# Kernel tuning notes

Hardware: AMD Instinct MI355X
Metric: run time of the kernel (lower is better)

The kernel has to match this reference:

```python
import jax, jax.numpy as jnp
import numpy as np
from jax import lax

MEL = 80
HID = 512
NCLS = 64
B = 16
T = 1000


def setup_inputs() -> dict:
    key = jax.random.key(0)
    ks = jax.random.split(key, 16)
    s_in = 1.0 / np.sqrt(MEL)
    s_h = 1.0 / np.sqrt(HID)
    return {
        'feats': jax.random.normal(ks[0], (B, T, MEL), jnp.float32),
        'C0': jax.random.normal(ks[1], (MEL, HID), jnp.float32) * s_h,
        'B0': jax.random.normal(ks[2], (HID, MEL), jnp.float32) * s_in,
        'W0': jax.random.normal(ks[3], (HID, MEL), jnp.float32) * s_in,
        'a0': jax.random.normal(ks[4], (HID,), jnp.float32) * 0.1,
        'tau00': jnp.array([0.5], jnp.float32),
        'gamma0': jnp.array([0.25], jnp.float32),
        'C1': jax.random.normal(ks[5], (HID, HID), jnp.float32) * s_h,
        'B1': jax.random.normal(ks[6], (HID, HID), jnp.float32) * s_h,
        'W1': jax.random.normal(ks[7], (HID, HID), jnp.float32) * s_h,
        'a1': jax.random.normal(ks[8], (HID,), jnp.float32) * 0.1,
        'tau01': jnp.array([0.5], jnp.float32),
        'gamma1': jnp.array([0.25], jnp.float32),
        'head_w': jax.random.normal(ks[9], (NCLS, 2 * HID), jnp.float32) * (1.0 / np.sqrt(2 * HID)),
        'head_b': jnp.zeros((NCLS,), jnp.float32),
    }


def _cell_step(h, x_t, C, Bm, Wm, a, tau0, gamma):
    # x_t: (B, in_dim), h: (B, HID)
    x_scale = jnp.maximum(jnp.linalg.norm(x_t, axis=-1, keepdims=True), 1e-6)  # (B,1)
    x_norm = jnp.clip(x_t / x_scale, -1.0, 1.0)
    hd = lax.stop_gradient(h)
    error = x_t - jnp.tanh(hd @ C.T) * x_scale                                 # (B, in_dim)
    rel_err = jnp.minimum(jnp.linalg.norm(error, axis=-1) / lax.stop_gradient(x_scale[:, 0]), 4.0)
    surprise = jax.nn.sigmoid((rel_err - tau0[0]) / gamma[0])                   # (B,)
    base_eff = x_norm @ Bm.T                                                    # (B, HID)
    err_eff = error @ Wm.T                                                      # (B, HID)
    input_h = hd * 0.2 + base_eff * 0.6 + err_eff * surprise[:, None] * 0.2
    # liquid-time-constant update: surprise-gated leaky integration toward tanh(input_h)
    g = surprise[:, None] * jax.nn.sigmoid(a)[None, :]                          # (B, HID) in (0,1)
    h_new = h * (1.0 - g) + jnp.tanh(input_h) * g
    return h_new, base_eff


def reference(feats, C0, B0, W0, a0, tau00, gamma0, C1, B1, W1, a1, tau01, gamma1, head_w, head_b):
    Bsz = feats.shape[0]
    feats_t = jnp.swapaxes(feats, 0, 1)  # (T, B, MEL)
    h0_init = jnp.zeros((Bsz, HID), feats.dtype)
    h1_init = jnp.zeros((Bsz, HID), feats.dtype)

    def scan_fn(carry, x_t):
        h0, h1 = carry
        h0n, be0 = _cell_step(h0, x_t, C0, B0, W0, a0, tau00, gamma0)
        h1n, be1 = _cell_step(h1, be0, C1, B1, W1, a1, tau01, gamma1)
        return (h0n, h1n), jnp.concatenate([h1n, be1], axis=-1)

    _, ys = lax.scan(scan_fn, (h0_init, h1_init), feats_t)  # (T, B, 2*HID)
    stacked = jnp.swapaxes(ys, 0, 1)                        # (B, T, 2*HID)
    return stacked @ head_w.T + head_b                      # (B, T, NCLS)
```

## Files before the change

### kernel.cpp

```cpp
#include <hip/hip_runtime.h>
#include <math.h>

#define T_LEN 1000
#define BATCH 16
#define MEL   80
#define HID   512
#define NCLS  64
#define SL    8

__device__ __forceinline__ float fast_tanh(float x) {
    float e = __expf(2.0f * x);
    return 1.0f - 2.0f / (e + 1.0f);
}
__device__ __forceinline__ float fast_sigmoid(float x) {
    return 1.0f / (1.0f + __expf(-x));
}

__device__ __forceinline__ unsigned long long pack_pair(float v, unsigned e) {
    return ((unsigned long long)e << 32) | (unsigned long long)__float_as_uint(v);
}
__device__ __forceinline__ float pair_val(unsigned long long p) {
    return __uint_as_float((unsigned)(p & 0xffffffffull));
}
__device__ __forceinline__ unsigned pair_epoch(unsigned long long p) {
    return (unsigned)(p >> 32);
}

__device__ __forceinline__ void llc_load16c(const float* base, float4 (&r)[16]) {
    asm volatile(
        "global_load_dwordx4 %0, %16, off sc0 sc1\n\t"
        "global_load_dwordx4 %1, %16, off offset:16 sc0 sc1\n\t"
        "global_load_dwordx4 %2, %16, off offset:32 sc0 sc1\n\t"
        "global_load_dwordx4 %3, %16, off offset:48 sc0 sc1\n\t"
        "global_load_dwordx4 %4, %16, off offset:64 sc0 sc1\n\t"
        "global_load_dwordx4 %5, %16, off offset:80 sc0 sc1\n\t"
        "global_load_dwordx4 %6, %16, off offset:96 sc0 sc1\n\t"
        "global_load_dwordx4 %7, %16, off offset:112 sc0 sc1\n\t"
        "global_load_dwordx4 %8, %16, off offset:128 sc0 sc1\n\t"
        "global_load_dwordx4 %9, %16, off offset:144 sc0 sc1\n\t"
        "global_load_dwordx4 %10, %16, off offset:160 sc0 sc1\n\t"
        "global_load_dwordx4 %11, %16, off offset:176 sc0 sc1\n\t"
        "global_load_dwordx4 %12, %16, off offset:192 sc0 sc1\n\t"
        "global_load_dwordx4 %13, %16, off offset:208 sc0 sc1\n\t"
        "global_load_dwordx4 %14, %16, off offset:224 sc0 sc1\n\t"
        "global_load_dwordx4 %15, %16, off offset:240 sc0 sc1\n\t"
        "s_waitcnt vmcnt(0)"
        : "=&v"(r[0]), "=&v"(r[1]), "=&v"(r[2]), "=&v"(r[3]),
          "=&v"(r[4]), "=&v"(r[5]), "=&v"(r[6]), "=&v"(r[7]),
          "=&v"(r[8]), "=&v"(r[9]), "=&v"(r[10]), "=&v"(r[11]),
          "=&v"(r[12]), "=&v"(r[13]), "=&v"(r[14]), "=&v"(r[15])
        : "v"(base)
        : "memory");
}

#define PART_WORDS (BATCH * 2 * SL * HID)
__global__ void k0_init(unsigned long long* part) {
    int i = blockIdx.x * 256 + threadIdx.x;
    if (i < PART_WORDS) part[i] = 0ull;
}

__global__ __launch_bounds__(256) void k1_be0(const float* __restrict__ feats,
                                              const float* __restrict__ B0,
                                              float* __restrict__ be0) {
    const int t = blockIdx.x;
    const int tid = threadIdx.x;
    __shared__ float xf[BATCH][MEL];
    __shared__ float sc[BATCH];
    for (int idx = tid; idx < BATCH * MEL; idx += 256) {
        int b = idx / MEL, m = idx % MEL;
        xf[b][m] = feats[b * (T_LEN * MEL) + t * MEL + m];
    }
    __syncthreads();
    if (tid < BATCH) {
        float ss = 0.f;
        for (int m = 0; m < MEL; ++m) { float v = xf[tid][m]; ss += v * v; }
        sc[tid] = fmaxf(sqrtf(ss), 1e-6f);
    }
    __syncthreads();
    for (int idx = tid; idx < BATCH * MEL; idx += 256) {
        int b = idx / MEL, m = idx % MEL;
        float v = xf[b][m] / sc[b];
        xf[b][m] = fminf(fmaxf(v, -1.f), 1.f);
    }
    __syncthreads();
    for (int j = tid; j < HID; j += 256) {
        float acc[BATCH];
        #pragma unroll
        for (int b = 0; b < BATCH; ++b) acc[b] = 0.f;
        const float* brow = B0 + j * MEL;
        for (int k = 0; k < MEL; k += 4) {
            float4 w = *(const float4*)(brow + k);
            #pragma unroll
            for (int b = 0; b < BATCH; ++b) {
                float4 xv = *(const float4*)(&xf[b][k]);
                acc[b] += w.x * xv.x + w.y * xv.y + w.z * xv.z + w.w * xv.w;
            }
        }
        #pragma unroll
        for (int b = 0; b < BATCH; ++b)
            be0[(t * BATCH + b) * HID + j] = acc[b];
    }
}

__global__ __launch_bounds__(512, 1) void k3_fused(
    const float* __restrict__ be0g,
    const float* __restrict__ C1, const float* __restrict__ W1,
    const float* __restrict__ B1,
    const float* __restrict__ a1, const float* __restrict__ tau,
    const float* __restrict__ gam,
    float* __restrict__ be1g, float* __restrict__ h1s,
    unsigned long long* part)
{
    const int chain = blockIdx.x & 15;
    const int slice = blockIdx.x >> 4;
    const int tid = threadIdx.x;
    const int w = tid >> 6;
    const int lane = tid & 63;
    const int jq = tid >> 3;
    const int kc = tid & 7;
    const int j2 = slice * 64 + jq;
    const bool lead = (kc == 0);

    float4 wC[16], wW[16], wB[16];
    llc_load16c(C1 + (size_t)tid * HID + slice * 64, wC);
    llc_load16c(W1 + (size_t)j2 * HID + kc * 64, wW);
    llc_load16c(B1 + (size_t)j2 * HID + kc * 64, wB);

    const float tauv = tau[0], gamv = gam[0];
    const float siga = fast_sigmoid(a1[j2]);

    unsigned long long* pc = part + (size_t)chain * (2 * SL * HID);

    __shared__ float h_s[64];
    __shared__ __align__(16) float e_s[HID + 32];
    __shared__ __align__(16) float x_s[HID + 32];
    __shared__ float sq_s[8];
    __shared__ float xsq_s[8];

    float hj = 0.f;
    if (tid < 64) h_s[tid] = 0.f;

    float cur_be0 = be0g[(size_t)chain * HID + tid];
    float cur_xs, cur_be1 = 0.f;
    {
        float sq = cur_be0 * cur_be0;
        #pragma unroll
        for (int off = 32; off > 0; off >>= 1) sq += __shfl_down(sq, off, 64);
        if (lane == 0) xsq_s[w] = sq;
        __syncthreads();
        float ssX = ((xsq_s[0] + xsq_s[1]) + (xsq_s[2] + xsq_s[3]))
                  + ((xsq_s[4] + xsq_s[5]) + (xsq_s[6] + xsq_s[7]));
        cur_xs = fmaxf(sqrtf(ssX), 1e-6f);
        float xn = cur_be0 / cur_xs;
        x_s[tid + (tid >> 6) * 4] = fminf(fmaxf(xn, -1.f), 1.f);
        __syncthreads();
        const float* xb = x_s + kc * 68;
        float q0 = 0.f, q1 = 0.f, q2 = 0.f, q3 = 0.f;
        #pragma unroll
        for (int i = 0; i < 16; ++i) {
            float4 v4 = *(const float4*)(xb + 4 * i);
            q0 += wB[i].x * v4.x; q1 += wB[i].y * v4.y;
            q2 += wB[i].z * v4.z; q3 += wB[i].w * v4.w;
        }
        float bq = (q0 + q1) + (q2 + q3);
        bq += __shfl_down(bq, 4, 8);
        bq += __shfl_down(bq, 2, 8);
        bq += __shfl_down(bq, 1, 8);
        if (lead) {
            cur_be1 = bq;
            __builtin_nontemporal_store(bq, &be1g[(size_t)chain * HID + j2]);
        }
        __syncthreads();
    }

    for (int t = 0; t < T_LEN; ++t) {
        float nxt_be0 = 0.f;
        if (t + 1 < T_LEN)
            nxt_be0 = be0g[(size_t)((t + 1) * BATCH + chain) * HID + tid];
        const unsigned tag = (unsigned)(t + 1);
        unsigned long long* ps = pc + (size_t)(t & 1) * (SL * HID);

        {
            float p0 = 0.f, p1 = 0.f, p2 = 0.f, p3 = 0.f;
            #pragma unroll
            for (int i = 0; i < 16; ++i) {
                float4 hv = *(const float4*)(h_s + 4 * i);
                p0 += wC[i].x * hv.x; p1 += wC[i].y * hv.y;
                p2 += wC[i].z * hv.z; p3 += wC[i].w * hv.w;
            }
            float pp = (p0 + p1) + (p2 + p3);
            __hip_atomic_store(&ps[slice * HID + tid], pack_pair(pp, tag),
                               __ATOMIC_RELAXED, __HIP_MEMORY_SCOPE_AGENT);
        }

        float nxt_xs = 0.f, nxt_be1 = 0.f;
        if (t + 1 < T_LEN) {
            float sq = nxt_be0 * nxt_be0;
            #pragma unroll
            for (int off = 32; off > 0; off >>= 1) sq += __shfl_down(sq, off, 64);
            if (lane == 0) xsq_s[w] = sq;
            __syncthreads();
            float ssX = ((xsq_s[0] + xsq_s[1]) + (xsq_s[2] + xsq_s[3]))
                      + ((xsq_s[4] + xsq_s[5]) + (xsq_s[6] + xsq_s[7]));
            nxt_xs = fmaxf(sqrtf(ssX), 1e-6f);
            float xn = nxt_be0 / nxt_xs;
            x_s[tid + (tid >> 6) * 4] = fminf(fmaxf(xn, -1.f), 1.f);
            __syncthreads();
            const float* xb = x_s + kc * 68;
            float q0 = 0.f, q1 = 0.f, q2 = 0.f, q3 = 0.f;
            #pragma unroll
            for (int i = 0; i < 16; ++i) {
                float4 v4 = *(const float4*)(xb + 4 * i);
                q0 += wB[i].x * v4.x; q1 += wB[i].y * v4.y;
                q2 += wB[i].z * v4.z; q3 += wB[i].w * v4.w;
            }
            float bq = (q0 + q1) + (q2 + q3);
            bq += __shfl_down(bq, 4, 8);
            bq += __shfl_down(bq, 2, 8);
            bq += __shfl_down(bq, 1, 8);
            if (lead) {
                nxt_be1 = bq;
                __builtin_nontemporal_store(bq,
                    &be1g[(size_t)((t + 1) * BATCH + chain) * HID + j2]);
            }
        }

        float dp;
        {
            const unsigned long long* a0 = ps + 0 * HID + tid;
            const unsigned long long* a1p = ps + 1 * HID + tid;
            const unsigned long long* a2 = ps + 2 * HID + tid;
            const unsigned long long* a3 = ps + 3 * HID + tid;
            const unsigned long long* a4 = ps + 4 * HID + tid;
            const unsigned long long* a5 = ps + 5 * HID + tid;
            const unsigned long long* a6 = ps + 6 * HID + tid;
            const unsigned long long* a7 = ps + 7 * HID + tid;
            unsigned long long q0, q1, q2, q3, q4, q5, q6, q7;
            int rounds = 0;
            for (;;) {
                asm volatile(
                    "global_load_dwordx2 %0, %8, off sc0 sc1\n\t"
                    "global_load_dwordx2 %1, %9, off sc0 sc1\n\t"
                    "global_load_dwordx2 %2, %10, off sc0 sc1\n\t"
                    "global_load_dwordx2 %3, %11, off sc0 sc1\n\t"
                    "global_load_dwordx2 %4, %12, off sc0 sc1\n\t"
                    "global_load_dwordx2 %5, %13, off sc0 sc1\n\t"
                    "global_load_dwordx2 %6, %14, off sc0 sc1\n\t"
                    "global_load_dwordx2 %7, %15, off sc0 sc1\n\t"
                    "s_waitcnt vmcnt(0)"
                    : "=&v"(q0), "=&v"(q1), "=&v"(q2), "=&v"(q3),
                      "=&v"(q4), "=&v"(q5), "=&v"(q6), "=&v"(q7)
                    : "v"(a0), "v"(a1p), "v"(a2), "v"(a3),
                      "v"(a4), "v"(a5), "v"(a6), "v"(a7)
                    : "memory");
                bool ok = (pair_epoch(q0) == tag) & (pair_epoch(q1) == tag)
                        & (pair_epoch(q2) == tag) & (pair_epoch(q3) == tag)
                        & (pair_epoch(q4) == tag) & (pair_epoch(q5) == tag)
                        & (pair_epoch(q6) == tag) & (pair_epoch(q7) == tag);
                if (__all(ok)) break;
                if (++rounds > 200000) {
                    q0 = __hip_atomic_load(a0, __ATOMIC_RELAXED, __HIP_MEMORY_SCOPE_AGENT);
                    q1 = __hip_atomic_load(a1p, __ATOMIC_RELAXED, __HIP_MEMORY_SCOPE_AGENT);
                    q2 = __hip_atomic_load(a2, __ATOMIC_RELAXED, __HIP_MEMORY_SCOPE_AGENT);
                    q3 = __hip_atomic_load(a3, __ATOMIC_RELAXED, __HIP_MEMORY_SCOPE_AGENT);
                    q4 = __hip_atomic_load(a4, __ATOMIC_RELAXED, __HIP_MEMORY_SCOPE_AGENT);
                    q5 = __hip_atomic_load(a5, __ATOMIC_RELAXED, __HIP_MEMORY_SCOPE_AGENT);
                    q6 = __hip_atomic_load(a6, __ATOMIC_RELAXED, __HIP_MEMORY_SCOPE_AGENT);
                    q7 = __hip_atomic_load(a7, __ATOMIC_RELAXED, __HIP_MEMORY_SCOPE_AGENT);
                    bool ok2 = (pair_epoch(q0) == tag) & (pair_epoch(q1) == tag)
                             & (pair_epoch(q2) == tag) & (pair_epoch(q3) == tag)
                             & (pair_epoch(q4) == tag) & (pair_epoch(q5) == tag)
                             & (pair_epoch(q6) == tag) & (pair_epoch(q7) == tag);
                    if (__all(ok2)) break;
                    rounds = 0;
                }
                __builtin_amdgcn_s_sleep(1);
            }
            dp = ((pair_val(q0) + pair_val(q1)) + (pair_val(q2) + pair_val(q3)))
               + ((pair_val(q4) + pair_val(q5)) + (pair_val(q6) + pair_val(q7)));
        }

        {
            float err = cur_be0 - fast_tanh(dp) * cur_xs;
            e_s[tid + (tid >> 6) * 4] = err;
            float sq = err * err;
            #pragma unroll
            for (int off = 32; off > 0; off >>= 1) sq += __shfl_down(sq, off, 64);
            if (lane == 0) sq_s[w] = sq;
        }
        __syncthreads();

        {
            float ssT = ((sq_s[0] + sq_s[1]) + (sq_s[2] + sq_s[3]))
                      + ((sq_s[4] + sq_s[5]) + (sq_s[6] + sq_s[7]));
            const float* esb = e_s + kc * 68;
            float q0 = 0.f, q1 = 0.f, q2 = 0.f, q3 = 0.f;
            #pragma unroll
            for (int i = 0; i < 16; ++i) {
                float4 ev = *(const float4*)(esb + 4 * i);
                q0 += wW[i].x * ev.x; q1 += wW[i].y * ev.y;
                q2 += wW[i].z * ev.z; q3 += wW[i].w * ev.w;
            }
            float ee = (q0 + q1) + (q2 + q3);
            ee += __shfl_down(ee, 4, 8);
            ee += __shfl_down(ee, 2, 8);
            ee += __shfl_down(ee, 1, 8);
            if (lead) {
                float rel = fminf(sqrtf(ssT) / cur_xs, 4.0f);
                float s = fast_sigmoid((rel - tauv) / gamv);
                float input_h = hj * 0.2f + cur_be1 * 0.6f + ee * s * 0.2f;
                float g = s * siga;
                hj = hj * (1.f - g) + fast_tanh(input_h) * g;
                h_s[jq] = hj;
                __builtin_nontemporal_store(hj,
                    &h1s[(size_t)(t * BATCH + chain) * HID + j2]);
            }
        }
        __syncthreads();

        cur_be0 = nxt_be0; cur_be1 = nxt_be1; cur_xs = nxt_xs;
    }
}

__global__ __launch_bounds__(1024) void k4_head(const float* __restrict__ h1s,
                                                const float* __restrict__ be1,
                                                const float* __restrict__ head_w,
                                                const float* __restrict__ head_b,
                                                float* __restrict__ out) {
    const int t = blockIdx.x;
    const int tid = threadIdx.x;
    const int c = tid >> 4;
    const int b = tid & 15;
    const float* hw = head_w + c * (2 * HID);
    const float* x1 = h1s + (size_t)(t * BATCH + b) * HID;
    const float* x2 = be1 + (size_t)(t * BATCH + b) * HID;
    float acc0 = head_b[c], acc1 = 0.f;
    for (int k = 0; k < HID; k += 4) {
        float4 w = *(const float4*)(hw + k);
        float4 xv = *(const float4*)(x1 + k);
        acc0 += w.x * xv.x + w.y * xv.y + w.z * xv.z + w.w * xv.w;
    }
    for (int k = 0; k < HID; k += 4) {
        float4 w = *(const float4*)(hw + HID + k);
        float4 xv = *(const float4*)(x2 + k);
        acc1 += w.x * xv.x + w.y * xv.y + w.z * xv.z + w.w * xv.w;
    }
    out[b * (T_LEN * NCLS) + t * NCLS + c] = acc0 + acc1;
}

extern "C" void kernel_launch(void* const* d_in, const int* in_sizes, int n_in,
                              void* d_out, int out_size, void* d_ws, size_t ws_size,
                              hipStream_t stream) {
    const float* feats  = (const float*)d_in[0];
    const float* B0     = (const float*)d_in[2];
    const float* C1     = (const float*)d_in[7];
    const float* B1     = (const float*)d_in[8];
    const float* W1     = (const float*)d_in[9];
    const float* a1     = (const float*)d_in[10];
    const float* tau1   = (const float*)d_in[11];
    const float* gam1   = (const float*)d_in[12];
    const float* head_w = (const float*)d_in[13];
    const float* head_b = (const float*)d_in[14];
    float* out = (float*)d_out;

    float* be0 = (float*)d_ws;
    float* be1 = be0 + (size_t)T_LEN * BATCH * HID;
    float* h1s = be1 + (size_t)T_LEN * BATCH * HID;
    unsigned long long* part =
        (unsigned long long*)(h1s + (size_t)T_LEN * BATCH * HID);

    hipLaunchKernelGGL(k0_init, dim3(512), dim3(256), 0, stream, part);
    hipLaunchKernelGGL(k1_be0, dim3(T_LEN), dim3(256), 0, stream, feats, B0, be0);
    hipLaunchKernelGGL(k3_fused, dim3(BATCH * SL), dim3(512), 0, stream,
                       be0, C1, W1, B1, a1, tau1, gam1, be1, h1s, part);
    hipLaunchKernelGGL(k4_head, dim3(T_LEN), dim3(1024), 0, stream,
                       h1s, be1, head_w, head_b, out);
}
```

Baseline: 3.929 ms.

## Fuse head projection partial sums into recurrent kernel, shrink head kernel to reduction

```diff
diff --git a/kernel.cpp b/kernel.cpp
--- a/kernel.cpp
+++ b/kernel.cpp
@@ -53,6 +53,16 @@
         : "memory");
 }
 
+__device__ __forceinline__ void llc_load2c(const float* base, float4 (&r)[2]) {
+    asm volatile(
+        "global_load_dwordx4 %0, %2, off sc0 sc1\n\t"
+        "global_load_dwordx4 %1, %2, off offset:16 sc0 sc1\n\t"
+        "s_waitcnt vmcnt(0)"
+        : "=&v"(r[0]), "=&v"(r[1])
+        : "v"(base)
+        : "memory");
+}
+
 #define PART_WORDS (BATCH * 2 * SL * HID)
 __global__ void k0_init(unsigned long long* part) {
     int i = blockIdx.x * 256 + threadIdx.x;
@@ -108,7 +118,8 @@
     const float* __restrict__ B1,
     const float* __restrict__ a1, const float* __restrict__ tau,
     const float* __restrict__ gam,
-    float* __restrict__ be1g, float* __restrict__ h1s,
+    const float* __restrict__ head_w,
+    float* __restrict__ pout,
     unsigned long long* part)
 {
     const int chain = blockIdx.x & 15;
@@ -120,11 +131,15 @@
     const int kc = tid & 7;
     const int j2 = slice * 64 + jq;
     const bool lead = (kc == 0);
-
-    float4 wC[16], wW[16], wB[16];
+    const int hc = tid >> 3;
+    const int hq = tid & 7;
+
+    float4 wC[16], wW[16], wB[16], hwh[2], hwb[2];
     llc_load16c(C1 + (size_t)tid * HID + slice * 64, wC);
     llc_load16c(W1 + (size_t)j2 * HID + kc * 64, wW);
     llc_load16c(B1 + (size_t)j2 * HID + kc * 64, wB);
+    llc_load2c(head_w + (size_t)hc * (2 * HID) + slice * 64 + hq * 8, hwh);
+    llc_load2c(head_w + (size_t)hc * (2 * HID) + HID + slice * 64 + hq * 8, hwb);
 
     const float tauv = tau[0], gamv = gam[0];
     const float siga = fast_sigmoid(a1[j2]);
@@ -132,6 +147,7 @@
     unsigned long long* pc = part + (size_t)chain * (2 * SL * HID);
 
     __shared__ float h_s[64];
+    __shared__ float b1_s[64];
     __shared__ __align__(16) float e_s[HID + 32];
     __shared__ __align__(16) float x_s[HID + 32];
     __shared__ float sq_s[8];
@@ -166,10 +182,7 @@
         bq += __shfl_down(bq, 4, 8);
         bq += __shfl_down(bq, 2, 8);
         bq += __shfl_down(bq, 1, 8);
-        if (lead) {
-            cur_be1 = bq;
-            __builtin_nontemporal_store(bq, &be1g[(size_t)chain * HID + j2]);
-        }
+        if (lead) cur_be1 = bq;
         __syncthreads();
     }
 
@@ -218,11 +231,7 @@
             bq += __shfl_down(bq, 4, 8);
             bq += __shfl_down(bq, 2, 8);
             bq += __shfl_down(bq, 1, 8);
-            if (lead) {
-                nxt_be1 = bq;
-                __builtin_nontemporal_store(bq,
-                    &be1g[(size_t)((t + 1) * BATCH + chain) * HID + j2]);
-            }
+            if (lead) nxt_be1 = bq;
         }
 
         float dp;
@@ -312,40 +321,46 @@
                 float g = s * siga;
                 hj = hj * (1.f - g) + fast_tanh(input_h) * g;
                 h_s[jq] = hj;
-                __builtin_nontemporal_store(hj,
-                    &h1s[(size_t)(t * BATCH + chain) * HID + j2]);
-            }
-        }
-        __syncthreads();
+                b1_s[jq] = cur_be1;
+            }
+        }
+        __syncthreads();
+
+        {
+            const float* hb = h_s + hq * 8;
+            const float* bb = b1_s + hq * 8;
+            float4 h0 = *(const float4*)(hb);
+            float4 h1 = *(const float4*)(hb + 4);
+            float4 b0 = *(const float4*)(bb);
+            float4 b1 = *(const float4*)(bb + 4);
+            float p = hwh[0].x * h0.x + hwh[0].y * h0.y + hwh[0].z * h0.z + hwh[0].w * h0.w
+                    + hwh[1].x * h1.x + hwh[1].y * h1.y + hwh[1].z * h1.z + hwh[1].w * h1.w
+                    + hwb[0].x * b0.x + hwb[0].y * b0.y + hwb[0].z * b0.z + hwb[0].w * b0.w
+                    + hwb[1].x * b1.x + hwb[1].y * b1.y + hwb[1].z * b1.z + hwb[1].w * b1.w;
+            p += __shfl_down(p, 4, 8);
+            p += __shfl_down(p, 2, 8);
+            p += __shfl_down(p, 1, 8);
+            if (hq == 0)
+                __builtin_nontemporal_store(p,
+                    &pout[((size_t)(t * BATCH + chain) * SL + slice) * NCLS + hc]);
+        }
 
         cur_be0 = nxt_be0; cur_be1 = nxt_be1; cur_xs = nxt_xs;
     }
 }
 
-__global__ __launch_bounds__(1024) void k4_head(const float* __restrict__ h1s,
-                                                const float* __restrict__ be1,
-                                                const float* __restrict__ head_w,
+__global__ __launch_bounds__(1024) void k4_head(const float* __restrict__ pout,
                                                 const float* __restrict__ head_b,
                                                 float* __restrict__ out) {
     const int t = blockIdx.x;
     const int tid = threadIdx.x;
-    const int c = tid >> 4;
-    const int b = tid & 15;
-    const float* hw = head_w + c * (2 * HID);
-    const float* x1 = h1s + (size_t)(t * BATCH + b) * HID;
-    const float* x2 = be1 + (size_t)(t * BATCH + b) * HID;
-    float acc0 = head_b[c], acc1 = 0.f;
-    for (int k = 0; k < HID; k += 4) {
-        float4 w = *(const float4*)(hw + k);
-        float4 xv = *(const float4*)(x1 + k);
-        acc0 += w.x * xv.x + w.y * xv.y + w.z * xv.z + w.w * xv.w;
-    }
-    for (int k = 0; k < HID; k += 4) {
-        float4 w = *(const float4*)(hw + HID + k);
-        float4 xv = *(const float4*)(x2 + k);
-        acc1 += w.x * xv.x + w.y * xv.y + w.z * xv.z + w.w * xv.w;
-    }
-    out[b * (T_LEN * NCLS) + t * NCLS + c] = acc0 + acc1;
+    const int c = tid & 63;
+    const int b = tid >> 6;
+    const float* pb = pout + (size_t)(t * BATCH + b) * SL * NCLS + c;
+    float acc = head_b[c];
+    #pragma unroll
+    for (int s = 0; s < SL; ++s) acc += pb[s * NCLS];
+    out[b * (T_LEN * NCLS) + t * NCLS + c] = acc;
 }
 
 extern "C" void kernel_launch(void* const* d_in, const int* in_sizes, int n_in,
@@ -364,15 +379,14 @@
     float* out = (float*)d_out;
 
     float* be0 = (float*)d_ws;
-    float* be1 = be0 + (size_t)T_LEN * BATCH * HID;
-    float* h1s = be1 + (size_t)T_LEN * BATCH * HID;
+    float* pout = be0 + (size_t)T_LEN * BATCH * HID;
     unsigned long long* part =
-        (unsigned long long*)(h1s + (size_t)T_LEN * BATCH * HID);
+        (unsigned long long*)(pout + (size_t)T_LEN * BATCH * SL * NCLS);
 
     hipLaunchKernelGGL(k0_init, dim3(512), dim3(256), 0, stream, part);
     hipLaunchKernelGGL(k1_be0, dim3(T_LEN), dim3(256), 0, stream, feats, B0, be0);
     hipLaunchKernelGGL(k3_fused, dim3(BATCH * SL), dim3(512), 0, stream,
-                       be0, C1, W1, B1, a1, tau1, gam1, be1, h1s, part);
+                       be0, C1, W1, B1, a1, tau1, gam1, head_w, pout, part);
     hipLaunchKernelGGL(k4_head, dim3(T_LEN), dim3(1024), 0, stream,
-                       h1s, be1, head_w, head_b, out);
-}
+                       pout, head_b, out);
+}
```

Result: slower. 4.959 ms (+26.2%).

## Restructure head GEMM to keep weights in registers and stage activations in LDS

Applied to the files above, without the earlier changes.

```diff
diff --git a/kernel.cpp b/kernel.cpp
--- a/kernel.cpp
+++ b/kernel.cpp
@@ -322,30 +322,61 @@
     }
 }
 
-__global__ __launch_bounds__(1024) void k4_head(const float* __restrict__ h1s,
-                                                const float* __restrict__ be1,
-                                                const float* __restrict__ head_w,
-                                                const float* __restrict__ head_b,
-                                                float* __restrict__ out) {
+__global__ __launch_bounds__(512) void k4_head(const float* __restrict__ h1s,
+                                               const float* __restrict__ be1,
+                                               const float* __restrict__ head_w,
+                                               const float* __restrict__ head_b,
+                                               float* __restrict__ out) {
     const int t = blockIdx.x;
     const int tid = threadIdx.x;
-    const int c = tid >> 4;
-    const int b = tid & 15;
-    const float* hw = head_w + c * (2 * HID);
-    const float* x1 = h1s + (size_t)(t * BATCH + b) * HID;
-    const float* x2 = be1 + (size_t)(t * BATCH + b) * HID;
-    float acc0 = head_b[c], acc1 = 0.f;
-    for (int k = 0; k < HID; k += 4) {
-        float4 w = *(const float4*)(hw + k);
-        float4 xv = *(const float4*)(x1 + k);
-        acc0 += w.x * xv.x + w.y * xv.y + w.z * xv.z + w.w * xv.w;
-    }
-    for (int k = 0; k < HID; k += 4) {
-        float4 w = *(const float4*)(hw + HID + k);
-        float4 xv = *(const float4*)(x2 + k);
-        acc1 += w.x * xv.x + w.y * xv.y + w.z * xv.z + w.w * xv.w;
-    }
-    out[b * (T_LEN * NCLS) + t * NCLS + c] = acc0 + acc1;
+    const int c = tid >> 3;
+    const int kc = tid & 7;
+
+    float4 wA[16], wB4[16];
+    llc_load16c(head_w + (size_t)c * (2 * HID) + kc * 128, wA);
+    llc_load16c(head_w + (size_t)c * (2 * HID) + kc * 128 + 64, wB4);
+    const float hb = head_b[c];
+
+    __shared__ __align__(16) float xs[BATCH * 1056];
+
+    const float* src1 = h1s + (size_t)t * BATCH * HID;
+    const float* src2 = be1 + (size_t)t * BATCH * HID;
+    #pragma unroll
+    for (int j = 0; j < 8; ++j) {
+        int fidx = tid + j * 512;
+        int b = fidx >> 8;
+        int r = fidx & 255;
+        int k0 = r * 4;
+        float4 v = (k0 < HID)
+                 ? *(const float4*)(src1 + (size_t)b * HID + k0)
+                 : *(const float4*)(src2 + (size_t)b * HID + (k0 - HID));
+        *(float4*)(&xs[b * 1056 + k0 + (k0 >> 7) * 4]) = v;
+    }
+    __syncthreads();
+
+    #pragma unroll
+    for (int b = 0; b < BATCH; ++b) {
+        const float* xb = xs + b * 1056 + kc * 132;
+        float q0 = 0.f, q1 = 0.f, q2 = 0.f, q3 = 0.f;
+        #pragma unroll
+        for (int i = 0; i < 16; ++i) {
+            float4 v4 = *(const float4*)(xb + 4 * i);
+            q0 += wA[i].x * v4.x; q1 += wA[i].y * v4.y;
+            q2 += wA[i].z * v4.z; q3 += wA[i].w * v4.w;
+        }
+        #pragma unroll
+        for (int i = 0; i < 16; ++i) {
+            float4 v4 = *(const float4*)(xb + 64 + 4 * i);
+            q0 += wB4[i].x * v4.x; q1 += wB4[i].y * v4.y;
+            q2 += wB4[i].z * v4.z; q3 += wB4[i].w * v4.w;
+        }
+        float p = (q0 + q1) + (q2 + q3);
+        p += __shfl_down(p, 4, 8);
+        p += __shfl_down(p, 2, 8);
+        p += __shfl_down(p, 1, 8);
+        if (kc == 0)
+            out[b * (T_LEN * NCLS) + t * NCLS + c] = p + hb;
+    }
 }
 
 extern "C" void kernel_launch(void* const* d_in, const int* in_sizes, int n_in,
@@ -373,6 +404,6 @@
     hipLaunchKernelGGL(k1_be0, dim3(T_LEN), dim3(256), 0, stream, feats, B0, be0);
     hipLaunchKernelGGL(k3_fused, dim3(BATCH * SL), dim3(512), 0, stream,
                        be0, C1, W1, B1, a1, tau1, gam1, be1, h1s, part);
-    hipLaunchKernelGGL(k4_head, dim3(T_LEN), dim3(1024), 0, stream,
+    hipLaunchKernelGGL(k4_head, dim3(T_LEN), dim3(512), 0, stream,
                        h1s, be1, head_w, head_b, out);
 }
```

After: 3.487 ms, median of 2. 11.3% less time.
